# Kernel optimization log

Hardware: AMD Instinct MI355X
Metric: run time of the kernel (lower is better)

Reference implementation:

```python
import jax, jax.numpy as jnp
import numpy as np


def setup_inputs() -> dict:
    key = jax.random.key(0)
    k1, k2, k3 = jax.random.split(key, 3)
    B, N, D, T = 8, 2, 256, 500
    SPK = 2000
    H = jax.random.normal(k1, (B, N, D, T), dtype=jnp.float32)
    S = jax.random.randint(k2, (B, N, T), 0, SPK, dtype=jnp.int64)
    E = jax.random.normal(k3, (SPK, D), dtype=jnp.float32)
    alpha = jnp.ones((1,), dtype=jnp.float32) * 10.0
    beta = jnp.ones((1,), dtype=jnp.float32) * 5.0
    return {"H": H, "S": S, "E": E, "alpha": alpha, "beta": beta, "N": 2}


def reference(H, S, E, alpha, beta, N):
    # H: (B, N, D, T); S: (B, N, T) int ids; E: (SPK, D)
    B, N_, D, T = H.shape
    # embedding lookup: (B, N, T, D) -> (B, N, D, T)
    E_S = jnp.transpose(E[S], (0, 1, 3, 2))
    # pairwise dist between predicted vectors and active-speaker embeddings
    # (B, N_pred=N, N_emb=N, T) -- small, direct broadcast
    Dist_p = jnp.sum((H[:, None, :, :, :] - E_S[:, :, None, :, :]) ** 2, axis=3)
    # N == 2 path matching (identity vs swap), min over the two alignments
    p0 = Dist_p[:, 0, 0, :] + Dist_p[:, 1, 1, :]  # (B, T)
    p1 = Dist_p[:, 0, 1, :] + Dist_p[:, 1, 0, :]  # (B, T)
    Dmin = jnp.minimum(p0, p1)                    # (B, T)
    Dmin = -alpha * Dmin + beta                   # broadcast (1,) over (B, T)
    # full distance to every speaker: ||H||^2 + ||E||^2 - 2 H.E
    # avoids materializing (B, SPK, N, D, T)
    Hsq = jnp.sum(H * H, axis=2)                  # (B, N, T)
    Esq = jnp.sum(E * E, axis=1)                  # (SPK,)
    cross = jnp.einsum('bndt,sd->bsnt', H, E)     # (B, SPK, N, T)
    Dist = Hsq[:, None, :, :] + Esq[None, :, None, None] - 2.0 * cross
    Dist = -alpha * Dist + beta                   # (B, SPK, N, T)
    lse = jax.nn.logsumexp(Dist, axis=1)          # (B, N, T)
    loss = -jnp.mean(Dmin) + jnp.mean(lse)
    return (E_S[:, :, :, 0], loss)
```

## Files before the change

### kernel.cpp

```cpp
#include <hip/hip_runtime.h>
#include <math.h>

#define Bb   8
#define Dd   256
#define Tt   500
#define SPK  2000
#define SPKP 2048
#define BN   16
#define L2E  1.4426950408889634f
#define LN2  0.6931471805599453f

#define EXP2F(x) __builtin_amdgcn_exp2f(x)
#define LOG2F(x) __builtin_amdgcn_logf(x)

#define F_ESN   0
#define F_HSQP  4096
#define F_PM    36864
#define F_PL    69632
#define F_DMP2  102400
#define EBF_BYTES ((size_t)167936 * 4)
#define HBF_BYTES (EBF_BYTES + (size_t)1048576)

#define ROWSTRIDE 264

typedef __bf16 v8bf __attribute__((ext_vector_type(8)));
typedef float  v4f  __attribute__((ext_vector_type(4)));

__device__ inline unsigned pack_bf16x2(float lo, float hi) {
    union { __bf16 h; unsigned short u; } a, b;
    a.h = (__bf16)lo; b.h = (__bf16)hi;
    return ((unsigned)b.u << 16) | (unsigned)a.u;
}

__global__ __launch_bounds__(256) void prep_all_kernel(
        const float* __restrict__ E, const int* __restrict__ S,
        const float* __restrict__ H, const float* __restrict__ alpha,
        const float* __restrict__ beta, float* __restrict__ ws,
        float* __restrict__ out) {
    int bid = blockIdx.x;
    int tid = threadIdx.x;

    if (bid < 512) {
        int s = bid * 4 + (tid >> 6);
        int lane = tid & 63;
        float4 v = make_float4(0.f, 0.f, 0.f, 0.f);
        if (s < SPK) v = ((const float4*)E)[s * 64 + lane];
        __bf16* ebf = (__bf16*)((char*)ws + EBF_BYTES);
        uint2 pp;
        pp.x = pack_bf16x2(v.x, v.y);
        pp.y = pack_bf16x2(v.z, v.w);
        *(uint2*)(ebf + (size_t)s * Dd + lane * 4) = pp;
        float acc = v.x * v.x + v.y * v.y + v.z * v.z + v.w * v.w;
        #pragma unroll
        for (int off = 32; off > 0; off >>= 1) acc += __shfl_down(acc, off, 64);
        if (lane == 0) ws[F_ESN + s] = (s < SPK) ? (-alpha[0] * acc * L2E) : -1e30f;
    } else if (bid < 528) {
        int i = (bid - 512) * 256 + tid;
        int bn = i >> 8, d = i & 255;
        out[i] = E[(size_t)S[bn * Tt] * Dd + d];
    } else {
        __shared__ float trans[32][65];
        int u = bid - 528;
        int bn = u >> 6;
        int r = u & 63;
        int tt0 = (r & 15) * 32;
        int d0 = (r >> 4) * 64;
        const float* Hb = H + (size_t)bn * Dd * Tt;
        #pragma unroll
        for (int rep = 0; rep < 2; ++rep) {
            int pair = rep * 256 + tid;
            int dd = pair >> 3;
            int tg = pair & 7;
            int t = tt0 + tg * 4;
            const float* src = Hb + (size_t)(d0 + dd) * Tt + t;
            float4 v;
            if (t + 3 < Tt) {
                v = *(const float4*)src;
            } else {
                v.x = (t + 0 < Tt) ? src[0] : 0.f;
                v.y = (t + 1 < Tt) ? src[1] : 0.f;
                v.z = (t + 2 < Tt) ? src[2] : 0.f;
                v.w = (t + 3 < Tt) ? src[3] : 0.f;
            }
            trans[tg * 4 + 0][dd] = v.x;
            trans[tg * 4 + 1][dd] = v.y;
            trans[tg * 4 + 2][dd] = v.z;
            trans[tg * 4 + 3][dd] = v.w;
        }
        __syncthreads();
        int tw = tid >> 3;
        int j = tid & 7;
        int t = tt0 + tw;
        bool ok = (t < Tt);
        int tc = ok ? t : (Tt - 1);
        int b = bn >> 1;
        int s0 = S[(b * 2 + 0) * Tt + tc];
        int s1 = S[(b * 2 + 1) * Tt + tc];
        const float4* e0p = (const float4*)(E + (size_t)s0 * Dd + d0 + j * 8);
        const float4* e1p = (const float4*)(E + (size_t)s1 * Dd + d0 + j * 8);
        float4 ea0 = e0p[0], ea1 = e0p[1];
        float4 eb0 = e1p[0], eb1 = e1p[1];
        float ev0[8] = {ea0.x, ea0.y, ea0.z, ea0.w, ea1.x, ea1.y, ea1.z, ea1.w};
        float ev1[8] = {eb0.x, eb0.y, eb0.z, eb0.w, eb1.x, eb1.y, eb1.z, eb1.w};
        float sq = 0.f, p0 = 0.f, p1 = 0.f;
        float vals[8];
        #pragma unroll
        for (int e = 0; e < 8; ++e) {
            float x = trans[tw][j * 8 + e];
            vals[e] = x;
            sq = fmaf(x, x, sq);
            float u0 = x - ev0[e]; p0 = fmaf(u0, u0, p0);
            float u1 = x - ev1[e]; p1 = fmaf(u1, u1, p1);
        }
        sq += __shfl_xor(sq, 1, 64); p0 += __shfl_xor(p0, 1, 64); p1 += __shfl_xor(p1, 1, 64);
        sq += __shfl_xor(sq, 2, 64); p0 += __shfl_xor(p0, 2, 64); p1 += __shfl_xor(p1, 2, 64);
        sq += __shfl_xor(sq, 4, 64); p0 += __shfl_xor(p0, 4, 64); p1 += __shfl_xor(p1, 4, 64);
        uint4 pk;
        pk.x = pack_bf16x2(vals[0], vals[1]);
        pk.y = pack_bf16x2(vals[2], vals[3]);
        pk.z = pack_bf16x2(vals[4], vals[5]);
        pk.w = pack_bf16x2(vals[6], vals[7]);
        __bf16* hbf = (__bf16*)((char*)ws + HBF_BYTES);
        *(uint4*)(hbf + ((size_t)(bn * 512 + t) * Dd + d0 + j * 8)) = pk;
        if (j == 0) {
            ws[F_HSQP + (size_t)(bn * 512 + t) * 4 + (r >> 4)] = sq;
            if (ok) {
                float2 pr = make_float2(p0, p1);
                *(float2*)(ws + F_DMP2 + (((size_t)bn * 512 + t) * 4 + (r >> 4)) * 2) = pr;
            }
        }
    }
}

__global__ __launch_bounds__(256, 2) void lse_mfma_kernel(
        const float* __restrict__ alpha, const float* __restrict__ beta,
        float* __restrict__ ws) {
    __shared__ __bf16 shB[64 * ROWSTRIDE];
    __shared__ float mrg_m[4][4][16], mrg_l[4][4][16];

    int bn = blockIdx.x;
    int t0 = blockIdx.y * 64;
    int mz = blockIdx.z;
    int tid = threadIdx.x;
    int lane = tid & 63;
    int n = lane & 15;
    int q = lane >> 4;
    int w = tid >> 6;

    const __bf16* ebf = (const __bf16*)((const char*)ws + EBF_BYTES);
    const __bf16* hbf = (const __bf16*)((const char*)ws + HBF_BYTES);

    #pragma unroll
    for (int p = 0; p < 8; ++p) {
        int flat = p * 256 + tid;
        int row = flat >> 5;
        int ch = flat & 31;
        uint4 vb = *(const uint4*)(hbf + ((size_t)(bn * 512 + t0 + row) * Dd + ch * 8));
        *(uint4*)(shB + row * ROWSTRIDE + ch * 8) = vb;
    }
    __syncthreads();

    v8bf bq[4][8];
    #pragma unroll
    for (int i = 0; i < 4; ++i) {
        int tloc = 16 * i + n;
        #pragma unroll
        for (int ks = 0; ks < 8; ++ks) {
            bq[i][ks] = *reinterpret_cast<const v8bf*>(&shB[tloc * ROWSTRIDE + ks * 32 + q * 8]);
        }
    }

    float A = alpha[0], Bv = beta[0];
    float ta2p = 2.f * A * L2E;
    float ctc2[4];
    #pragma unroll
    for (int i = 0; i < 4; ++i) {
        int t = t0 + 16 * i + n;
        float4 hq = *(const float4*)(ws + F_HSQP + (size_t)(bn * 512 + t) * 4);
        float hs = hq.x + hq.y + hq.z + hq.w;
        ctc2[i] = (t < Tt) ? ((Bv - A * hs) * L2E) : 0.f;
    }

    float lm[4], ll[4];
    #pragma unroll
    for (int i = 0; i < 4; ++i) { lm[i] = -INFINITY; ll[i] = 0.f; }

    const __bf16* ap = ebf + ((size_t)(mz * 512 + w * 16 + n) * Dd) + q * 8;
    const float* esb = ws + F_ESN + mz * 512 + w * 16 + q * 4;

    #pragma unroll
    for (int c = 0; c < 8; ++c) {
        v8bf af[8];
        #pragma unroll
        for (int ks = 0; ks < 8; ++ks) {
            af[ks] = *reinterpret_cast<const v8bf*>(ap + (size_t)c * 64 * Dd + ks * 32);
        }
        float4 es4 = *(const float4*)(esb + c * 64);

        v4f acc[4];
        #pragma unroll
        for (int i = 0; i < 4; ++i) acc[i] = (v4f){0.f, 0.f, 0.f, 0.f};
        #pragma unroll
        for (int ks = 0; ks < 8; ++ks) {
            #pragma unroll
            for (int i = 0; i < 4; ++i) {
                acc[i] = __builtin_amdgcn_mfma_f32_16x16x32_bf16(af[ks], bq[i][ks], acc[i], 0, 0, 0);
            }
        }
        float e0 = es4.x, e1 = es4.y, e2 = es4.z, e3 = es4.w;
        #pragma unroll
        for (int i = 0; i < 4; ++i) {
            float c2 = ctc2[i];
            float v0 = fmaf(ta2p, acc[i][0], c2 + e0);
            float v1 = fmaf(ta2p, acc[i][1], c2 + e1);
            float v2 = fmaf(ta2p, acc[i][2], c2 + e2);
            float v3 = fmaf(ta2p, acc[i][3], c2 + e3);
            float vm = fmaxf(fmaxf(v0, v1), fmaxf(v2, v3));
            float s = EXP2F(v0 - vm) + EXP2F(v1 - vm) + EXP2F(v2 - vm) + EXP2F(v3 - vm);
            float nm = fmaxf(lm[i], vm);
            ll[i] = ll[i] * EXP2F(lm[i] - nm) + s * EXP2F(vm - nm);
            lm[i] = nm;
        }
    }

    #pragma unroll
    for (int i = 0; i < 4; ++i) {
        float m = lm[i], l = ll[i];
        #pragma unroll
        for (int msk = 16; msk <= 32; msk <<= 1) {
            float om = __shfl_xor(m, msk, 64);
            float ol = __shfl_xor(l, msk, 64);
            float nm = fmaxf(m, om);
            l = l * EXP2F(m - nm) + ol * EXP2F(om - nm);
            m = nm;
        }
        if (q == 0) { mrg_m[w][i][n] = m; mrg_l[w][i][n] = l; }
    }
    __syncthreads();

    if (tid < 64) {
        int i = tid >> 4, cc = tid & 15;
        float m = mrg_m[0][i][cc], l = mrg_l[0][i][cc];
        #pragma unroll
        for (int wv = 1; wv < 4; ++wv) {
            float om = mrg_m[wv][i][cc], ol = mrg_l[wv][i][cc];
            float nm = fmaxf(m, om);
            l = l * EXP2F(m - nm) + ol * EXP2F(om - nm);
            m = nm;
        }
        int tw = t0 + 16 * i + cc;
        if (tw < Tt) {
            ws[F_PM + (bn * 512 + tw) * 4 + mz] = m;
            ws[F_PL + (bn * 512 + tw) * 4 + mz] = l;
        }
    }
}

__global__ __launch_bounds__(1024) void final_kernel(
        const float* __restrict__ alpha, const float* __restrict__ beta,
        const float* __restrict__ ws, float* __restrict__ out) {
    __shared__ float rL[16], rD[16];
    int tid = threadIdx.x;
    float A = alpha[0], Bv = beta[0];

    float lsum = 0.f;
    #pragma unroll
    for (int it = 0; it < 8; ++it) {
        int idx = it * 1024 + tid;
        int t = idx & 511;
        if (t < Tt) {
            int base = idx * 4;
            float4 m4 = *(const float4*)(ws + F_PM + base);
            float4 l4 = *(const float4*)(ws + F_PL + base);
            float m = m4.x, l = l4.x, nm;
            nm = fmaxf(m, m4.y); l = l * EXP2F(m - nm) + l4.y * EXP2F(m4.y - nm); m = nm;
            nm = fmaxf(m, m4.z); l = l * EXP2F(m - nm) + l4.z * EXP2F(m4.z - nm); m = nm;
            nm = fmaxf(m, m4.w); l = l * EXP2F(m - nm) + l4.w * EXP2F(m4.w - nm); m = nm;
            lsum += LN2 * (m + LOG2F(l));
        }
    }

    float dsum = 0.f;
    #pragma unroll
    for (int it = 0; it < 4; ++it) {
        int idx = it * 1024 + tid;
        int t = idx & 511;
        if (t < Tt) {
            int b = idx >> 9;
            const float4* P0 = (const float4*)(ws + F_DMP2 + ((size_t)(2 * b + 0) * 512 + t) * 8);
            const float4* P1 = (const float4*)(ws + F_DMP2 + ((size_t)(2 * b + 1) * 512 + t) * 8);
            float4 a0 = P0[0], a1 = P0[1];
            float4 b0 = P1[0], b1 = P1[1];
            float d00 = a0.x + a0.z + a1.x + a1.z;
            float d01 = a0.y + a0.w + a1.y + a1.w;
            float d10 = b0.x + b0.z + b1.x + b1.z;
            float d11 = b0.y + b0.w + b1.y + b1.w;
            float dm = fminf(d00 + d11, d01 + d10);
            dsum += -A * dm + Bv;
        }
    }

    int lane = tid & 63, w = tid >> 6;
    #pragma unroll
    for (int off = 32; off > 0; off >>= 1) {
        lsum += __shfl_down(lsum, off, 64);
        dsum += __shfl_down(dsum, off, 64);
    }
    if (lane == 0) { rL[w] = lsum; rD[w] = dsum; }
    __syncthreads();
    if (tid == 0) {
        float L = 0.f, D = 0.f;
        #pragma unroll
        for (int wv = 0; wv < 16; ++wv) { L += rL[wv]; D += rD[wv]; }
        out[BN * Dd] = -(D / (float)(Bb * Tt)) + L / (float)(BN * Tt);
    }
}

extern "C" void kernel_launch(void* const* d_in, const int* in_sizes, int n_in,
                              void* d_out, int out_size, void* d_ws, size_t ws_size,
                              hipStream_t stream) {
    const float* H     = (const float*)d_in[0];
    const int*   S     = (const int*)d_in[1];
    const float* E     = (const float*)d_in[2];
    const float* alpha = (const float*)d_in[3];
    const float* beta  = (const float*)d_in[4];
    float* out = (float*)d_out;
    float* ws  = (float*)d_ws;

    prep_all_kernel<<<1552, 256, 0, stream>>>(E, S, H, alpha, beta, ws, out);
    lse_mfma_kernel<<<dim3(BN, 8, 4), 256, 0, stream>>>(alpha, beta, ws);
    final_kernel<<<1, 1024, 0, stream>>>(alpha, beta, ws, out);
}
```

Baseline: 107.8 us.

## Split speaker dimension across 8 blocks and stream B fragments from LDS

The LSE MFMA kernel now splits the 2048 padded speakers into 8 chunks instead of 4, doubling the grid to 1024 blocks. Each block loops 4 times instead of 8, and partial max/sum results are stored with stride 8; the final kernel merges 8 partials. B fragments are reloaded from shared memory inside the MFMA loop instead of being held in 32 v8bf registers, which lowers register pressure and should raise occupancy at the cost of more LDS traffic. The H transpose in the prep kernel is also changed from float4 loads to scalar coalesced loads.

```diff
diff --git a/kernel.cpp b/kernel.cpp
--- a/kernel.cpp
+++ b/kernel.cpp
@@ -16,9 +16,9 @@
 #define F_ESN   0
 #define F_HSQP  4096
 #define F_PM    36864
-#define F_PL    69632
-#define F_DMP2  102400
-#define EBF_BYTES ((size_t)167936 * 4)
+#define F_PL    102400
+#define F_DMP2  167936
+#define EBF_BYTES ((size_t)233472 * 4)
 #define HBF_BYTES (EBF_BYTES + (size_t)1048576)
 
 #define ROWSTRIDE 264
@@ -67,25 +67,12 @@
         int d0 = (r >> 4) * 64;
         const float* Hb = H + (size_t)bn * Dd * Tt;
         #pragma unroll
-        for (int rep = 0; rep < 2; ++rep) {
-            int pair = rep * 256 + tid;
-            int dd = pair >> 3;
-            int tg = pair & 7;
-            int t = tt0 + tg * 4;
-            const float* src = Hb + (size_t)(d0 + dd) * Tt + t;
-            float4 v;
-            if (t + 3 < Tt) {
-                v = *(const float4*)src;
-            } else {
-                v.x = (t + 0 < Tt) ? src[0] : 0.f;
-                v.y = (t + 1 < Tt) ? src[1] : 0.f;
-                v.z = (t + 2 < Tt) ? src[2] : 0.f;
-                v.w = (t + 3 < Tt) ? src[3] : 0.f;
-            }
-            trans[tg * 4 + 0][dd] = v.x;
-            trans[tg * 4 + 1][dd] = v.y;
-            trans[tg * 4 + 2][dd] = v.z;
-            trans[tg * 4 + 3][dd] = v.w;
+        for (int p = 0; p < 8; ++p) {
+            int flat = p * 256 + tid;
+            int dd = flat >> 5;
+            int tl = flat & 31;
+            int t = tt0 + tl;
+            trans[tl][dd] = (t < Tt) ? Hb[(size_t)(d0 + dd) * Tt + t] : 0.f;
         }
         __syncthreads();
         int tw = tid >> 3;
@@ -160,16 +147,6 @@
     }
     __syncthreads();
 
-    v8bf bq[4][8];
-    #pragma unroll
-    for (int i = 0; i < 4; ++i) {
-        int tloc = 16 * i + n;
-        #pragma unroll
-        for (int ks = 0; ks < 8; ++ks) {
-            bq[i][ks] = *reinterpret_cast<const v8bf*>(&shB[tloc * ROWSTRIDE + ks * 32 + q * 8]);
-        }
-    }
-
     float A = alpha[0], Bv = beta[0];
     float ta2p = 2.f * A * L2E;
     float ctc2[4];
@@ -185,11 +162,10 @@
     #pragma unroll
     for (int i = 0; i < 4; ++i) { lm[i] = -INFINITY; ll[i] = 0.f; }
 
-    const __bf16* ap = ebf + ((size_t)(mz * 512 + w * 16 + n) * Dd) + q * 8;
-    const float* esb = ws + F_ESN + mz * 512 + w * 16 + q * 4;
-
-    #pragma unroll
-    for (int c = 0; c < 8; ++c) {
+    const __bf16* ap = ebf + ((size_t)(mz * 256 + w * 16 + n) * Dd) + q * 8;
+    const float* esb = ws + F_ESN + mz * 256 + w * 16 + q * 4;
+
+    for (int c = 0; c < 4; ++c) {
         v8bf af[8];
         #pragma unroll
         for (int ks = 0; ks < 8; ++ks) {
@@ -204,7 +180,9 @@
         for (int ks = 0; ks < 8; ++ks) {
             #pragma unroll
             for (int i = 0; i < 4; ++i) {
-                acc[i] = __builtin_amdgcn_mfma_f32_16x16x32_bf16(af[ks], bq[i][ks], acc[i], 0, 0, 0);
+                v8bf bqv = *reinterpret_cast<const v8bf*>(
+                    &shB[(16 * i + n) * ROWSTRIDE + ks * 32 + q * 8]);
+                acc[i] = __builtin_amdgcn_mfma_f32_16x16x32_bf16(af[ks], bqv, acc[i], 0, 0, 0);
             }
         }
         float e0 = es4.x, e1 = es4.y, e2 = es4.z, e3 = es4.w;
@@ -250,8 +228,8 @@
         }
         int tw = t0 + 16 * i + cc;
         if (tw < Tt) {
-            ws[F_PM + (bn * 512 + tw) * 4 + mz] = m;
-            ws[F_PL + (bn * 512 + tw) * 4 + mz] = l;
+            ws[F_PM + ((size_t)(bn * 512 + tw)) * 8 + mz] = m;
+            ws[F_PL + ((size_t)(bn * 512 + tw)) * 8 + mz] = l;
         }
     }
 }
@@ -269,13 +247,18 @@
         int idx = it * 1024 + tid;
         int t = idx & 511;
         if (t < Tt) {
-            int base = idx * 4;
-            float4 m4 = *(const float4*)(ws + F_PM + base);
-            float4 l4 = *(const float4*)(ws + F_PL + base);
+            const float4* M = (const float4*)(ws + F_PM + (size_t)idx * 8);
+            const float4* L = (const float4*)(ws + F_PL + (size_t)idx * 8);
+            float4 m4 = M[0], m5 = M[1];
+            float4 l4 = L[0], l5 = L[1];
             float m = m4.x, l = l4.x, nm;
             nm = fmaxf(m, m4.y); l = l * EXP2F(m - nm) + l4.y * EXP2F(m4.y - nm); m = nm;
             nm = fmaxf(m, m4.z); l = l * EXP2F(m - nm) + l4.z * EXP2F(m4.z - nm); m = nm;
             nm = fmaxf(m, m4.w); l = l * EXP2F(m - nm) + l4.w * EXP2F(m4.w - nm); m = nm;
+            nm = fmaxf(m, m5.x); l = l * EXP2F(m - nm) + l5.x * EXP2F(m5.x - nm); m = nm;
+            nm = fmaxf(m, m5.y); l = l * EXP2F(m - nm) + l5.y * EXP2F(m5.y - nm); m = nm;
+            nm = fmaxf(m, m5.z); l = l * EXP2F(m - nm) + l5.z * EXP2F(m5.z - nm); m = nm;
+            nm = fmaxf(m, m5.w); l = l * EXP2F(m - nm) + l5.w * EXP2F(m5.w - nm); m = nm;
             lsum += LN2 * (m + LOG2F(l));
         }
     }
@@ -328,6 +311,6 @@
     float* ws  = (float*)d_ws;
 
     prep_all_kernel<<<1552, 256, 0, stream>>>(E, S, H, alpha, beta, ws, out);
-    lse_mfma_kernel<<<dim3(BN, 8, 4), 256, 0, stream>>>(alpha, beta, ws);
+    lse_mfma_kernel<<<dim3(BN, 8, 8), 256, 0, stream>>>(alpha, beta, ws);
     final_kernel<<<1, 1024, 0, stream>>>(alpha, beta, ws, out);
 }
```

New measurement: 108.7 us. No clear change (+0.8%).
